# Optimization experiments

Measured on AMD Instinct MI355X. Metric: run time of the kernel, lower is better.

Reference implementation:

```python
import jax, jax.numpy as jnp
import numpy as np

B = 16384    # batch of game states
HAND = 8     # max_hand_size
A = 30       # max_actions
C = 4        # max cards per action combo
E = 32       # card_embed_dim
HID = 128    # hidden_dim


def _encode_cards(cards, val_emb, suit_emb, type_emb):
    # cards: int array, 0 = padding, 53 = joker (treated as padding for value/suit)
    invalid = (cards == 0) | (cards == 53)
    values = jnp.where(invalid, 0, (cards - 1) % 13 + 1)
    suits = jnp.where(invalid, 0, (cards - 1) // 13 + 1)
    ce = jnp.concatenate([val_emb[values], suit_emb[suits]], axis=-1)  # [..., E]
    ct = jnp.where(values == 11, 1, jnp.where(values == 12, 2, jnp.where(values == 13, 3, 0)))
    te = type_emb[ct]  # [..., 8]
    pad = jnp.zeros(te.shape[:-1] + (E - te.shape[-1],), ce.dtype)
    return ce + jnp.concatenate([te, pad], axis=-1)


def _mha(q, kv, wq, bq, wk, bk, wv, bv, wo, bo, nh, kpm=None):
    b, sq, e = q.shape
    sk = kv.shape[1]
    hd = e // nh
    Q = (q @ wq + bq).reshape(b, sq, nh, hd)
    K = (kv @ wk + bk).reshape(b, sk, nh, hd)
    V = (kv @ wv + bv).reshape(b, sk, nh, hd)
    s = jnp.einsum('bqhd,bkhd->bhqk', Q, K) * (1.0 / np.sqrt(hd))
    if kpm is not None:  # kpm True = valid key
        s = s + jnp.where(kpm[:, None, None, :], 0.0, -1e9)
    a = jax.nn.softmax(s, axis=-1)
    o = jnp.einsum('bhqk,bkhd->bqhd', a, V).reshape(b, sq, e)
    return o @ wo + bo


def _combo_features(cards):
    # cards: [A, C] int, 0 = padding. Vectorized version of _compute_combo_features.
    mask = cards != 0
    combo_size = mask.sum(1).astype(jnp.float32)
    values = jnp.where(mask, (cards - 1) % 13 + 1, 0)
    has_valid = mask.any(1)
    fidx = jnp.argmax(mask, axis=1)
    fv = values[jnp.arange(cards.shape[0]), fidx]  # first valid value per action
    same = jnp.where(mask, values == fv[:, None], True).all(1).astype(jnp.float32)
    vf = values.astype(jnp.float32)
    attack = jnp.where(values == 1, 1.0,
             jnp.where(values == 11, 10.0,
             jnp.where(values == 12, 15.0,
             jnp.where(values == 13, 20.0, vf))))
    total = (attack * mask).sum(1)
    suits = jnp.where(mask, (cards - 1) // 13 + 1, 0)
    uniq = jnp.stack([(suits == s).any(1) for s in (1, 2, 3, 4)], 0).sum(0).astype(jnp.float32)
    ace = ((values == 1) & mask).any(1).astype(jnp.float32)
    valid = ((combo_size <= 4.0) & ((same > 0) | (ace > 0))).astype(jnp.float32)
    feats = jnp.stack([combo_size, same, total, uniq, ace, valid], axis=1)  # [A, 6]
    return jnp.where(has_valid[:, None], feats, 0.0), has_valid


def _forward(hand_cards, enemy_card, hand_size, game_state, discard_pile_cards,
             action_card_indices, num_valid_actions,
             val_emb, suit_emb, type_emb,
             ce_w1, ce_b1, ce_w2, ce_b2,
             ha_wq, ha_bq, ha_wk, ha_bk, ha_wv, ha_bv, ha_wo, ha_bo,
             he_wq, he_bq, he_wk, he_bk, he_wv, he_bv, he_wo, he_bo,
             se_w1, se_b1, se_w2, se_b2,
             atc_w1, atc_b1, atc_w2, atc_b2,
             as_w1, as_b1, as_w2, as_b2, as_w3, as_b3,
             cx_w1, cx_b1, cx_w2, cx_b2, cx_w3, cx_b3):
    relu = jax.nn.relu
    hand_emb = _encode_cards(hand_cards, val_emb, suit_emb, type_emb)            # [B, HAND, E]
    enemy_emb = _encode_cards(enemy_card[:, None], val_emb, suit_emb, type_emb)  # [B, 1, E]
    hand_mask = hand_cards != 0
    attended = _mha(hand_emb, hand_emb, ha_wq, ha_bq, ha_wk, ha_bk, ha_wv, ha_bv, ha_wo, ha_bo, 8, kpm=hand_mask)
    ctx_he = _mha(attended, enemy_emb, he_wq, he_bq, he_wk, he_bk, he_wv, he_bv, he_wo, he_bo, 4)
    lengths = jnp.maximum(hand_size.astype(jnp.float32), 1.0)[:, None]
    hand_ctx = ctx_he.sum(1) / lengths                                           # [B, E]

    # strategic features (batched per game state)
    hvals = jnp.where(hand_cards == 0, 0, (hand_cards - 1) % 13 + 1)
    hsz = hand_size.astype(jnp.float32)
    aces = (hvals == 1).sum(1).astype(jnp.float32)
    faces = ((hvals >= 11) & (hvals <= 13)).sum(1).astype(jnp.float32)
    low = ((hvals >= 2) & (hvals <= 6)).sum(1).astype(jnp.float32)
    hsuits = jnp.where(hand_cards == 0, 0, (hand_cards - 1) // 13 + 1)
    scnt = [(hsuits == s).sum(1).astype(jnp.float32) for s in (1, 2, 3, 4)]
    hvr = faces / (hsz + 1e-8)
    sdiv = jnp.stack([(hsuits == s).any(1) for s in (1, 2, 3, 4)], 0).sum(0).astype(jnp.float32) / 4.0
    strat = jnp.stack([hsz, aces, faces, low, scnt[0], scnt[1], scnt[2], scnt[3], hvr, sdiv], axis=1)
    strat_in = jnp.concatenate([game_state, strat], axis=1)                      # [B, 20]
    strat_ctx = relu(strat_in @ se_w1 + se_b1) @ se_w2 + se_b2                   # [B, 32]

    combined = jnp.concatenate([hand_ctx, enemy_emb[:, 0], strat_ctx, discard_pile_cards], axis=1)  # [B, 150]
    h = relu(combined @ cx_w1 + cx_b1)
    h = relu(h @ cx_w2 + cx_b2)
    ctx = h @ cx_w3 + cx_b3                                                      # [B, HID]
    type_probs = jax.nn.softmax(relu(ctx @ atc_w1 + atc_b1) @ atc_w2 + atc_b2, axis=-1)  # [B, 4]

    feats, has_valid = _combo_features(action_card_indices)                      # [A, 6], [A]
    emb = _encode_cards(action_card_indices, val_emb, suit_emb, type_emb)        # [A, C, E]
    m = (action_card_indices != 0).astype(emb.dtype)[..., None]
    cnt = jnp.maximum(m.sum(1), 1.0)
    act_emb = (emb * m).sum(1) / cnt                                             # masked mean over real cards
    act_emb = jnp.where(has_valid[:, None], act_emb, 0.0)
    combo_enc = relu(feats @ ce_w1 + ce_b1) @ ce_w2 + ce_b2                      # [A, 16]

    Bn = ctx.shape[0]
    af = jnp.concatenate([
        jnp.broadcast_to(ctx[:, None, :], (Bn, A, HID)),
        jnp.broadcast_to(act_emb[None], (Bn, A, E)),
        jnp.broadcast_to(combo_enc[None], (Bn, A, 16)),
    ], axis=-1)                                                                  # [B, A, 176]
    s = relu(af @ as_w1 + as_b1)
    s = relu(s @ as_w2 + as_b2)
    score = (s @ as_w3 + as_b3)[..., 0]                                          # [B, A]

    strength = feats[:, 2] / 20.0                                                # [A]
    bonus_valid = type_probs[:, 0:1] * strength[None, :] + type_probs[:, 1:2] * (1.0 - strength[None, :])
    bonus_empty = jnp.broadcast_to(type_probs[:, 3:4] * 2.0, (Bn, A))
    bonus = jnp.where(has_valid[None, :], bonus_valid, bonus_empty)
    return score + bonus                                                          # [B, A]


def setup_inputs() -> dict:
    key = jax.random.key(0)
    ki = iter(jax.random.split(key, 64))
    def nrm(shape, s):
        return (s * jax.random.normal(next(ki), shape)).astype(jnp.float32)
    def lin(i, o, s=0.08):
        return nrm((i, o), s), nrm((o,), 0.02)
    d = {}
    hc = jax.random.randint(next(ki), (B, HAND), 0, 53)
    d['hand_cards'] = hc.at[:, 0].set(jax.random.randint(next(ki), (B,), 1, 53))  # at least one valid card per hand
    d['enemy_card'] = jax.random.randint(next(ki), (B,), 1, 53)
    d['hand_size'] = jax.random.randint(next(ki), (B,), 1, 9)
    d['game_state'] = nrm((B, 10), 1.0)
    d['discard_pile_cards'] = jax.random.uniform(next(ki), (B, 54), dtype=jnp.float32)
    d['action_card_indices'] = jax.random.randint(next(ki), (A, C), 1, 53)
    d['num_valid_actions'] = A
    d['val_emb'] = nrm((14, 16), 0.1).at[0].set(0.0)   # padding_idx=0
    d['suit_emb'] = nrm((5, 16), 0.1).at[0].set(0.0)   # padding_idx=0
    d['type_emb'] = nrm((4, 8), 0.1)
    d['ce_w1'], d['ce_b1'] = lin(6, 32)
    d['ce_w2'], d['ce_b2'] = lin(32, 16)
    for p in ('ha', 'he'):
        for t in ('q', 'k', 'v', 'o'):
            d[p + '_w' + t], d[p + '_b' + t] = lin(E, E)
    d['se_w1'], d['se_b1'] = lin(20, 64)
    d['se_w2'], d['se_b2'] = lin(64, 32)
    d['atc_w1'], d['atc_b1'] = lin(HID, 64)
    d['atc_w2'], d['atc_b2'] = lin(64, 4)
    d['as_w1'], d['as_b1'] = lin(HID + E + 16, 64)
    d['as_w2'], d['as_b2'] = lin(64, 32)
    d['as_w3'], d['as_b3'] = lin(32, 1)
    d['cx_w1'], d['cx_b1'] = lin(2 * E + 32 + 54, HID)
    d['cx_w2'], d['cx_b2'] = lin(HID, HID)
    d['cx_w3'], d['cx_b3'] = lin(HID, HID)
    return d


def reference(hand_cards, enemy_card, hand_size, game_state, discard_pile_cards,
              action_card_indices, num_valid_actions,
              val_emb, suit_emb, type_emb,
              ce_w1, ce_b1, ce_w2, ce_b2,
              ha_wq, ha_bq, ha_wk, ha_bk, ha_wv, ha_bv, ha_wo, ha_bo,
              he_wq, he_bq, he_wk, he_bk, he_wv, he_bv, he_wo, he_bo,
              se_w1, se_b1, se_w2, se_b2,
              atc_w1, atc_b1, atc_w2, atc_b2,
              as_w1, as_b1, as_w2, as_b2, as_w3, as_b3,
              cx_w1, cx_b1, cx_w2, cx_b2, cx_w3, cx_b3):
    return _forward(hand_cards, enemy_card, hand_size, game_state, discard_pile_cards,
                    action_card_indices, num_valid_actions,
                    val_emb, suit_emb, type_emb,
                    ce_w1, ce_b1, ce_w2, ce_b2,
                    ha_wq, ha_bq, ha_wk, ha_bk, ha_wv, ha_bv, ha_wo, ha_bo,
                    he_wq, he_bq, he_wk, he_bk, he_wv, he_bv, he_wo, he_bo,
                    se_w1, se_b1, se_w2, se_b2,
                    atc_w1, atc_b1, atc_w2, atc_b2,
                    as_w1, as_b1, as_w2, as_b2, as_w3, as_b3,
                    cx_w1, cx_b1, cx_w2, cx_b2, cx_w3, cx_b3)
```

## Files before the change

kernel.cpp:

```cpp
#include <hip/hip_runtime.h>
#include <math.h>


__device__ __forceinline__ void encode_card32(int c,
                                              const float* __restrict__ val_emb,
                                              const float* __restrict__ suit_emb,
                                              const float* __restrict__ type_emb,
                                              float* e) {
  bool inv = (c == 0) || (c == 53);
  int v = inv ? 0 : ((c - 1) % 13 + 1);
  int s = inv ? 0 : ((c - 1) / 13 + 1);
  int ct = (v == 11) ? 1 : (v == 12) ? 2 : (v == 13) ? 3 : 0;
#pragma unroll
  for (int i = 0; i < 16; ++i) e[i] = val_emb[v * 16 + i];
#pragma unroll
  for (int i = 0; i < 16; ++i) e[16 + i] = suit_emb[s * 16 + i];
#pragma unroll
  for (int i = 0; i < 8; ++i) e[i] += type_emb[ct * 8 + i];
}

__global__ __launch_bounds__(64) void action_kernel(
    const int* __restrict__ acards,
    const float* __restrict__ val_emb, const float* __restrict__ suit_emb,
    const float* __restrict__ type_emb,
    const float* __restrict__ ce_w1, const float* __restrict__ ce_b1,
    const float* __restrict__ ce_w2, const float* __restrict__ ce_b2,
    const float* __restrict__ as_w1, const float* __restrict__ as_b1,
    float* __restrict__ ws) {
  __shared__ float sAct[30][32];
  __shared__ float sCombo[30][16];
  const int tid = threadIdx.x;

  if (tid < 30) {
    int c[4];
#pragma unroll
    for (int i = 0; i < 4; ++i) c[i] = acards[tid * 4 + i];
    bool mask[4]; int vals[4], suits[4]; int csize = 0; bool hasv = false;
#pragma unroll
    for (int i = 0; i < 4; ++i) {
      mask[i] = (c[i] != 0);
      if (mask[i]) { csize++; hasv = true; }
      vals[i] = mask[i] ? ((c[i] - 1) % 13 + 1) : 0;
      suits[i] = mask[i] ? ((c[i] - 1) / 13 + 1) : 0;
    }
    int fvv = mask[0] ? vals[0] : mask[1] ? vals[1] : mask[2] ? vals[2]
              : mask[3] ? vals[3] : vals[0];
    bool same = true;
#pragma unroll
    for (int i = 0; i < 4; ++i) if (mask[i] && vals[i] != fvv) same = false;
    float total = 0.f;
#pragma unroll
    for (int i = 0; i < 4; ++i) {
      if (mask[i]) {
        int v = vals[i];
        total += (v == 1) ? 1.f : (v == 11) ? 10.f : (v == 12) ? 15.f
                 : (v == 13) ? 20.f : (float)v;
      }
    }
    float uniq = 0.f;
#pragma unroll
    for (int s = 1; s <= 4; ++s) {
      bool any = false;
#pragma unroll
      for (int i = 0; i < 4; ++i) if (suits[i] == s) any = true;
      uniq += any ? 1.f : 0.f;
    }
    bool ace = false;
#pragma unroll
    for (int i = 0; i < 4; ++i) if (mask[i] && vals[i] == 1) ace = true;
    float f_same = same ? 1.f : 0.f, f_ace = ace ? 1.f : 0.f;
    float valid = (((float)csize <= 4.f) && (f_same > 0.f || f_ace > 0.f)) ? 1.f : 0.f;
    float feats[6] = {(float)csize, f_same, total, uniq, f_ace, valid};
    if (!hasv) { for (int i = 0; i < 6; ++i) feats[i] = 0.f; }
    float emb[32];
#pragma unroll
    for (int i = 0; i < 32; ++i) emb[i] = 0.f;
    float cnt = 0.f;
#pragma unroll
    for (int i = 0; i < 4; ++i) {
      float e[32];
      encode_card32(c[i], val_emb, suit_emb, type_emb, e);
      if (mask[i]) {
#pragma unroll
        for (int j = 0; j < 32; ++j) emb[j] += e[j];
        cnt += 1.f;
      }
    }
    float invc = 1.f / fmaxf(cnt, 1.f);
#pragma unroll
    for (int j = 0; j < 32; ++j) sAct[tid][j] = hasv ? emb[j] * invc : 0.f;
    float t32[32];
#pragma unroll
    for (int j = 0; j < 32; ++j) {
      float acc = ce_b1[j];
#pragma unroll
      for (int k = 0; k < 6; ++k) acc += feats[k] * ce_w1[k * 32 + j];
      t32[j] = fmaxf(acc, 0.f);
    }
#pragma unroll
    for (int j = 0; j < 16; ++j) {
      float acc = ce_b2[j];
#pragma unroll
      for (int k = 0; k < 32; ++k) acc += t32[k] * ce_w2[k * 16 + j];
      sCombo[tid][j] = acc;
    }
    ws[1920 + tid] = total * 0.05f;
    ws[1950 + tid] = hasv ? 1.f : 0.f;
  }
  __syncthreads();
  for (int idx = tid; idx < 1920; idx += 64) {
    int a = idx >> 6, j = idx & 63;
    float acc = as_b1[j];
#pragma unroll
    for (int k = 0; k < 32; ++k) acc += sAct[a][k] * as_w1[(128 + k) * 64 + j];
#pragma unroll
    for (int k = 0; k < 16; ++k) acc += sCombo[a][k] * as_w1[(160 + k) * 64 + j];
    ws[idx] = acc;
  }
}

template <int K, int NJ, bool RELU, bool HASB>
__device__ __forceinline__ void layerT(
    const float* __restrict__ inB, float* __restrict__ outB,
    const float* __restrict__ W, int ldw, int j0,
    const float* __restrict__ bias, int r) {
  float acc[NJ];
#pragma unroll
  for (int j = 0; j < NJ; ++j) acc[j] = HASB ? bias[j0 + j] : 0.f;
#pragma unroll 4
  for (int k = 0; k < K; ++k) {
    float a = inB[k * 64 + r];
    const float* wr = W + (size_t)k * ldw + j0;
#pragma unroll
    for (int j = 0; j < NJ; ++j) acc[j] += a * wr[j];
  }
#pragma unroll
  for (int j = 0; j < NJ; ++j)
    outB[(j0 + j) * 64 + r] = RELU ? fmaxf(acc[j], 0.f) : acc[j];
}

__global__ __launch_bounds__(1024) void policy_main(
    const int* __restrict__ hand_cards, const int* __restrict__ enemy_card,
    const int* __restrict__ hand_size, const float* __restrict__ game_state,
    const float* __restrict__ discard,
    const float* __restrict__ val_emb, const float* __restrict__ suit_emb,
    const float* __restrict__ type_emb,
    const float* __restrict__ he_wv, const float* __restrict__ he_bv,
    const float* __restrict__ he_wo, const float* __restrict__ he_bo,
    const float* __restrict__ se_w1, const float* __restrict__ se_b1,
    const float* __restrict__ se_w2, const float* __restrict__ se_b2,
    const float* __restrict__ atc_w1, const float* __restrict__ atc_b1,
    const float* __restrict__ atc_w2, const float* __restrict__ atc_b2,
    const float* __restrict__ as_w1,
    const float* __restrict__ as_w2, const float* __restrict__ as_b2,
    const float* __restrict__ as_w3, const float* __restrict__ as_b3,
    const float* __restrict__ cx_w1, const float* __restrict__ cx_b1,
    const float* __restrict__ cx_w2, const float* __restrict__ cx_b2,
    const float* __restrict__ cx_w3, const float* __restrict__ cx_b3,
    const float* __restrict__ ws, float* __restrict__ out) {
  __shared__ float bufA[128 * 64];
  __shared__ float bufB[128 * 64];

  const int tid = threadIdx.x;
  const int r = tid & 63;
  const int wq = __builtin_amdgcn_readfirstlane(tid >> 6);
  const int b0 = blockIdx.x * 64;

  if (wq == 2) {
#pragma unroll
    for (int k = 0; k < 10; ++k)
      bufB[k * 64 + r] = game_state[(size_t)(b0 + r) * 10 + k];
  }
  if (wq == 0) {
    const int b = b0 + r;
    const float hsz = (float)hand_size[b];
    int aces = 0, faces = 0, low = 0, c1 = 0, c2 = 0, c3 = 0, c4 = 0;
#pragma unroll
    for (int i = 0; i < 8; ++i) {
      int c = hand_cards[b * 8 + i];
      int v = (c == 0) ? 0 : ((c - 1) % 13 + 1);
      int s = (c == 0) ? 0 : ((c - 1) / 13 + 1);
      aces += (v == 1);
      faces += (v >= 11 && v <= 13);
      low += (v >= 2 && v <= 6);
      c1 += (s == 1); c2 += (s == 2); c3 += (s == 3); c4 += (s == 4);
    }
    float sdiv = (float)((c1 > 0) + (c2 > 0) + (c3 > 0) + (c4 > 0)) * 0.25f;
    float hvr = (float)faces / (hsz + 1e-8f);
    bufB[(10 + 0) * 64 + r] = hsz;          bufB[(10 + 1) * 64 + r] = (float)aces;
    bufB[(10 + 2) * 64 + r] = (float)faces; bufB[(10 + 3) * 64 + r] = (float)low;
    bufB[(10 + 4) * 64 + r] = (float)c1;    bufB[(10 + 5) * 64 + r] = (float)c2;
    bufB[(10 + 6) * 64 + r] = (float)c3;    bufB[(10 + 7) * 64 + r] = (float)c4;
    bufB[(10 + 8) * 64 + r] = hvr;          bufB[(10 + 9) * 64 + r] = sdiv;
  }
  if (wq == 1) {
    const int b = b0 + r;
    bufB[116 * 64 + r] = 8.0f / fmaxf((float)hand_size[b], 1.0f);
    float e[32];
    encode_card32(enemy_card[b], val_emb, suit_emb, type_emb, e);
#pragma unroll
    for (int i = 0; i < 32; ++i) bufA[(32 + i) * 64 + r] = e[i];
  }
  __syncthreads();

  layerT<20, 4, true, true>(bufB, bufB + 20 * 64, se_w1, 64, wq * 4, se_b1, r);
  __syncthreads();

  layerT<64, 2, false, true>(bufB + 20 * 64, bufA + 64 * 64, se_w2, 32, wq * 2, se_b2, r);
  layerT<32, 2, false, true>(bufA + 32 * 64, bufB + 84 * 64, he_wv, 32, wq * 2, he_bv, r);
  __syncthreads();

  {
    const int j0 = wq * 2;
    float acc[2] = {he_bo[j0], he_bo[j0 + 1]};
#pragma unroll 4
    for (int k = 0; k < 32; ++k) {
      float a = bufB[(84 + k) * 64 + r];
      const float* wr = he_wo + (size_t)k * 32 + j0;
      acc[0] += a * wr[0];
      acc[1] += a * wr[1];
    }
    float scale = bufB[116 * 64 + r];
    bufA[(j0 + 0) * 64 + r] = scale * acc[0];
    bufA[(j0 + 1) * 64 + r] = scale * acc[1];
  }
  __syncthreads();

  {
    const int j0 = wq * 8;
    float acc[8];
#pragma unroll
    for (int j = 0; j < 8; ++j) acc[j] = cx_b1[j0 + j];
#pragma unroll 4
    for (int k = 0; k < 96; ++k) {
      float a = bufA[k * 64 + r];
      const float* wr = cx_w1 + (size_t)k * 128 + j0;
#pragma unroll
      for (int j = 0; j < 8; ++j) acc[j] += a * wr[j];
    }
    const float* drow = discard + (size_t)(b0 + r) * 54;
#pragma unroll 2
    for (int k = 0; k < 54; ++k) {
      float a = drow[k];
      const float* wr = cx_w1 + (size_t)(96 + k) * 128 + j0;
#pragma unroll
      for (int j = 0; j < 8; ++j) acc[j] += a * wr[j];
    }
    __syncthreads();
#pragma unroll
    for (int j = 0; j < 8; ++j) bufB[(j0 + j) * 64 + r] = fmaxf(acc[j], 0.f);
  }
  __syncthreads();

  layerT<128, 8, true, true>(bufB, bufA, cx_w2, 128, wq * 8, cx_b2, r);
  __syncthreads();

  layerT<128, 8, false, true>(bufA, bufB, cx_w3, 128, wq * 8, cx_b3, r);
  __syncthreads();

  if (wq < 8) {
    layerT<128, 8, true, true>(bufB, bufA, atc_w1, 64, wq * 8, atc_b1, r);
  } else {
    layerT<128, 8, false, false>(bufB, bufA + 64 * 64, as_w1, 64, (wq - 8) * 8,
                                 nullptr, r);
  }
  __syncthreads();

  if (wq < 4) {
    float acc = atc_b2[wq];
#pragma unroll 4
    for (int k = 0; k < 64; ++k) acc += bufA[k * 64 + r] * atc_w2[k * 4 + wq];
    bufB[wq * 64 + r] = acc;
  }
  __syncthreads();

  if (wq < 15) {
    float l0 = bufB[0 * 64 + r], l1 = bufB[1 * 64 + r];
    float l2 = bufB[2 * 64 + r], l3 = bufB[3 * 64 + r];
    float m = fmaxf(fmaxf(l0, l1), fmaxf(l2, l3));
    float e0 = expf(l0 - m), e1 = expf(l1 - m), e2 = expf(l2 - m), e3 = expf(l3 - m);
    float inv = 1.f / (e0 + e1 + e2 + e3);
    float tp0 = e0 * inv, tp1 = e1 * inv, tp3 = e3 * inv;

    const float b3v = as_b3[0];
#pragma unroll 1
    for (int i = 0; i < 2; ++i) {
      const int a = wq * 2 + i;
      const float* qa = ws + a * 64;
      float acc[32];
#pragma unroll
      for (int j = 0; j < 32; ++j) acc[j] = 0.f;
#pragma unroll 1
      for (int seg = 0; seg < 4; ++seg) {
        float p[16];
#pragma unroll
        for (int kk = 0; kk < 16; ++kk)
          p[kk] = bufA[(64 + seg * 16 + kk) * 64 + r];
#pragma unroll
        for (int kk = 0; kk < 16; ++kk) {
          float s = fmaxf(p[kk] + qa[seg * 16 + kk], 0.f);
          const float* w2r = as_w2 + (size_t)(seg * 16 + kk) * 32;
#pragma unroll
          for (int j = 0; j < 32; ++j) acc[j] += s * w2r[j];
        }
      }
      float sc = b3v;
#pragma unroll
      for (int j = 0; j < 32; ++j)
        sc += fmaxf(acc[j] + as_b2[j], 0.f) * as_w3[j];
      float st = ws[1920 + a], hv = ws[1950 + a];
      float bon = (hv > 0.5f) ? (tp0 * st + tp1 * (1.f - st)) : tp3 * 2.f;
      out[(size_t)(b0 + r) * 30 + a] = sc + bon;
    }
  }
}

extern "C" void kernel_launch(void* const* d_in, const int* in_sizes, int n_in,
                              void* d_out, int out_size, void* d_ws, size_t ws_size,
                              hipStream_t stream) {
  (void)in_sizes; (void)n_in; (void)out_size; (void)ws_size;
  const int* hand_cards = (const int*)d_in[0];
  const int* enemy_card = (const int*)d_in[1];
  const int* hand_size = (const int*)d_in[2];
  const float* game_state = (const float*)d_in[3];
  const float* discard = (const float*)d_in[4];
  const int* acards = (const int*)d_in[5];
  const float* val_emb = (const float*)d_in[7];
  const float* suit_emb = (const float*)d_in[8];
  const float* type_emb = (const float*)d_in[9];
  const float* ce_w1 = (const float*)d_in[10], * ce_b1 = (const float*)d_in[11];
  const float* ce_w2 = (const float*)d_in[12], * ce_b2 = (const float*)d_in[13];
  const float* he_wv = (const float*)d_in[26], * he_bv = (const float*)d_in[27];
  const float* he_wo = (const float*)d_in[28], * he_bo = (const float*)d_in[29];
  const float* se_w1 = (const float*)d_in[30], * se_b1 = (const float*)d_in[31];
  const float* se_w2 = (const float*)d_in[32], * se_b2 = (const float*)d_in[33];
  const float* atc_w1 = (const float*)d_in[34], * atc_b1 = (const float*)d_in[35];
  const float* atc_w2 = (const float*)d_in[36], * atc_b2 = (const float*)d_in[37];
  const float* as_w1 = (const float*)d_in[38], * as_b1 = (const float*)d_in[39];
  const float* as_w2 = (const float*)d_in[40], * as_b2 = (const float*)d_in[41];
  const float* as_w3 = (const float*)d_in[42], * as_b3 = (const float*)d_in[43];
  const float* cx_w1 = (const float*)d_in[44], * cx_b1 = (const float*)d_in[45];
  const float* cx_w2 = (const float*)d_in[46], * cx_b2 = (const float*)d_in[47];
  const float* cx_w3 = (const float*)d_in[48], * cx_b3 = (const float*)d_in[49];
  float* ws = (float*)d_ws;
  float* out = (float*)d_out;

  hipLaunchKernelGGL(action_kernel, dim3(1), dim3(64), 0, stream,
                     acards, val_emb, suit_emb, type_emb,
                     ce_w1, ce_b1, ce_w2, ce_b2, as_w1, as_b1, ws);
  hipLaunchKernelGGL(policy_main, dim3(256), dim3(1024), 0, stream,
                     hand_cards, enemy_card, hand_size, game_state, discard,
                     val_emb, suit_emb, type_emb,
                     he_wv, he_bv, he_wo, he_bo,
                     se_w1, se_b1, se_w2, se_b2,
                     atc_w1, atc_b1, atc_w2, atc_b2,
                     as_w1, as_w2, as_b2, as_w3, as_b3,
                     cx_w1, cx_b1, cx_w2, cx_b2, cx_w3, cx_b3,
                     ws, out);
}
```

Baseline: 259.4 us.

## Store activations in quad-interleaved shared layout for float4 LDS access

Changes the shared-memory activation buffers from column-major [col][row] to a quad-interleaved layout, so each thread reads and writes four consecutive features as one float4. The aim is fewer LDS instructions in the MLP layers and the scoring loop. It also removes one barrier inside the cx layer-1 block and tidies the accumulator code. The cost is 16-byte LDS accesses, which may bring bank-conflict or alignment trade-offs, and more complex indexing that has to stay consistent across every stage.

```diff
diff --git a/kernel.cpp b/kernel.cpp
--- a/kernel.cpp
+++ b/kernel.cpp
@@ -1,6 +1,8 @@
 #include <hip/hip_runtime.h>
 #include <math.h>
 
+
+#define QOFF(c, r) ((((c) >> 2) * 256) + ((r) * 4) + ((c) & 3))
 
 __device__ __forceinline__ void encode_card32(int c,
                                               const float* __restrict__ val_emb,
@@ -119,24 +121,52 @@
   }
 }
 
-template <int K, int NJ, bool RELU, bool HASB>
-__device__ __forceinline__ void layerT(
-    const float* __restrict__ inB, float* __restrict__ outB,
-    const float* __restrict__ W, int ldw, int j0,
+template <int K, int NJ, bool RELU, bool HASB, bool QIN, bool QOUT>
+__device__ __forceinline__ void layerU(
+    const float* __restrict__ in, int inColBase, float* __restrict__ outB,
+    int outColBase, const float* __restrict__ W, int ldw, int j0,
     const float* __restrict__ bias, int r) {
   float acc[NJ];
 #pragma unroll
   for (int j = 0; j < NJ; ++j) acc[j] = HASB ? bias[j0 + j] : 0.f;
+  if constexpr (QIN) {
+    static_assert(K % 4 == 0, "quad input needs K%4==0");
+    const int g0 = inColBase >> 2;
 #pragma unroll 4
-  for (int k = 0; k < K; ++k) {
-    float a = inB[k * 64 + r];
-    const float* wr = W + (size_t)k * ldw + j0;
-#pragma unroll
-    for (int j = 0; j < NJ; ++j) acc[j] += a * wr[j];
-  }
-#pragma unroll
-  for (int j = 0; j < NJ; ++j)
-    outB[(j0 + j) * 64 + r] = RELU ? fmaxf(acc[j], 0.f) : acc[j];
+    for (int g = 0; g < K / 4; ++g) {
+      float4 a = *(const float4*)&in[(g0 + g) * 256 + r * 4];
+#pragma unroll
+      for (int q = 0; q < 4; ++q) {
+        float av = (q == 0) ? a.x : (q == 1) ? a.y : (q == 2) ? a.z : a.w;
+        const float* wr = W + (size_t)(g * 4 + q) * ldw + j0;
+#pragma unroll
+        for (int j = 0; j < NJ; ++j) acc[j] += av * wr[j];
+      }
+    }
+  } else {
+#pragma unroll 4
+    for (int k = 0; k < K; ++k) {
+      float a = in[(inColBase + k) * 64 + r];
+      const float* wr = W + (size_t)k * ldw + j0;
+#pragma unroll
+      for (int j = 0; j < NJ; ++j) acc[j] += a * wr[j];
+    }
+  }
+#pragma unroll
+  for (int j = 0; j < NJ; ++j) if (RELU) acc[j] = fmaxf(acc[j], 0.f);
+  if constexpr (QOUT && NJ == 8) {
+    const int c0 = outColBase + j0;
+    float4 o0 = make_float4(acc[0], acc[1], acc[2], acc[3]);
+    float4 o1 = make_float4(acc[4], acc[5], acc[6], acc[7]);
+    *(float4*)&outB[(c0 >> 2) * 256 + r * 4] = o0;
+    *(float4*)&outB[((c0 >> 2) + 1) * 256 + r * 4] = o1;
+  } else if constexpr (QOUT) {
+#pragma unroll
+    for (int j = 0; j < NJ; ++j) outB[QOFF(outColBase + j0 + j, r)] = acc[j];
+  } else {
+#pragma unroll
+    for (int j = 0; j < NJ; ++j) outB[(outColBase + j0 + j) * 64 + r] = acc[j];
+  }
 }
 
 __global__ __launch_bounds__(1024) void policy_main(
@@ -199,30 +229,36 @@
     float e[32];
     encode_card32(enemy_card[b], val_emb, suit_emb, type_emb, e);
 #pragma unroll
-    for (int i = 0; i < 32; ++i) bufA[(32 + i) * 64 + r] = e[i];
-  }
-  __syncthreads();
-
-  layerT<20, 4, true, true>(bufB, bufB + 20 * 64, se_w1, 64, wq * 4, se_b1, r);
-  __syncthreads();
-
-  layerT<64, 2, false, true>(bufB + 20 * 64, bufA + 64 * 64, se_w2, 32, wq * 2, se_b2, r);
-  layerT<32, 2, false, true>(bufA + 32 * 64, bufB + 84 * 64, he_wv, 32, wq * 2, he_bv, r);
+    for (int g = 0; g < 8; ++g) {
+      float4 ev = make_float4(e[g * 4], e[g * 4 + 1], e[g * 4 + 2], e[g * 4 + 3]);
+      *(float4*)&bufA[(8 + g) * 256 + r * 4] = ev;
+    }
+  }
+  __syncthreads();
+
+  layerU<20, 4, true, true, false, false>(bufB, 0, bufB, 20, se_w1, 64, wq * 4,
+                                          se_b1, r);
+  __syncthreads();
+
+  layerU<64, 2, false, true, false, true>(bufB, 20, bufA, 64, se_w2, 32, wq * 2,
+                                          se_b2, r);
+  layerU<32, 2, false, true, true, false>(bufA, 32, bufB, 84, he_wv, 32, wq * 2,
+                                          he_bv, r);
   __syncthreads();
 
   {
     const int j0 = wq * 2;
-    float acc[2] = {he_bo[j0], he_bo[j0 + 1]};
+    float acc0 = he_bo[j0], acc1 = he_bo[j0 + 1];
 #pragma unroll 4
     for (int k = 0; k < 32; ++k) {
       float a = bufB[(84 + k) * 64 + r];
       const float* wr = he_wo + (size_t)k * 32 + j0;
-      acc[0] += a * wr[0];
-      acc[1] += a * wr[1];
+      acc0 += a * wr[0];
+      acc1 += a * wr[1];
     }
     float scale = bufB[116 * 64 + r];
-    bufA[(j0 + 0) * 64 + r] = scale * acc[0];
-    bufA[(j0 + 1) * 64 + r] = scale * acc[1];
+    bufA[QOFF(j0, r)] = scale * acc0;
+    bufA[QOFF(j0 + 1, r)] = scale * acc1;
   }
   __syncthreads();
 
@@ -232,11 +268,15 @@
 #pragma unroll
     for (int j = 0; j < 8; ++j) acc[j] = cx_b1[j0 + j];
 #pragma unroll 4
-    for (int k = 0; k < 96; ++k) {
-      float a = bufA[k * 64 + r];
-      const float* wr = cx_w1 + (size_t)k * 128 + j0;
-#pragma unroll
-      for (int j = 0; j < 8; ++j) acc[j] += a * wr[j];
+    for (int g = 0; g < 24; ++g) {
+      float4 a = *(const float4*)&bufA[g * 256 + r * 4];
+#pragma unroll
+      for (int q = 0; q < 4; ++q) {
+        float av = (q == 0) ? a.x : (q == 1) ? a.y : (q == 2) ? a.z : a.w;
+        const float* wr = cx_w1 + (size_t)(g * 4 + q) * 128 + j0;
+#pragma unroll
+        for (int j = 0; j < 8; ++j) acc[j] += av * wr[j];
+      }
     }
     const float* drow = discard + (size_t)(b0 + r) * 54;
 #pragma unroll 2
@@ -246,30 +286,42 @@
 #pragma unroll
       for (int j = 0; j < 8; ++j) acc[j] += a * wr[j];
     }
-    __syncthreads();
-#pragma unroll
-    for (int j = 0; j < 8; ++j) bufB[(j0 + j) * 64 + r] = fmaxf(acc[j], 0.f);
-  }
-  __syncthreads();
-
-  layerT<128, 8, true, true>(bufB, bufA, cx_w2, 128, wq * 8, cx_b2, r);
-  __syncthreads();
-
-  layerT<128, 8, false, true>(bufA, bufB, cx_w3, 128, wq * 8, cx_b3, r);
+    float4 o0 = make_float4(fmaxf(acc[0], 0.f), fmaxf(acc[1], 0.f),
+                            fmaxf(acc[2], 0.f), fmaxf(acc[3], 0.f));
+    float4 o1 = make_float4(fmaxf(acc[4], 0.f), fmaxf(acc[5], 0.f),
+                            fmaxf(acc[6], 0.f), fmaxf(acc[7], 0.f));
+    *(float4*)&bufB[(j0 >> 2) * 256 + r * 4] = o0;
+    *(float4*)&bufB[((j0 >> 2) + 1) * 256 + r * 4] = o1;
+  }
+  __syncthreads();
+
+  layerU<128, 8, true, true, true, true>(bufB, 0, bufA, 0, cx_w2, 128, wq * 8,
+                                         cx_b2, r);
+  __syncthreads();
+
+  layerU<128, 8, false, true, true, true>(bufA, 0, bufB, 0, cx_w3, 128, wq * 8,
+                                          cx_b3, r);
   __syncthreads();
 
   if (wq < 8) {
-    layerT<128, 8, true, true>(bufB, bufA, atc_w1, 64, wq * 8, atc_b1, r);
+    layerU<128, 8, true, true, true, true>(bufB, 0, bufA, 0, atc_w1, 64, wq * 8,
+                                           atc_b1, r);
   } else {
-    layerT<128, 8, false, false>(bufB, bufA + 64 * 64, as_w1, 64, (wq - 8) * 8,
-                                 nullptr, r);
+    layerU<128, 8, false, false, true, true>(bufB, 0, bufA, 64, as_w1, 64,
+                                             (wq - 8) * 8, nullptr, r);
   }
   __syncthreads();
 
   if (wq < 4) {
     float acc = atc_b2[wq];
 #pragma unroll 4
-    for (int k = 0; k < 64; ++k) acc += bufA[k * 64 + r] * atc_w2[k * 4 + wq];
+    for (int g = 0; g < 16; ++g) {
+      float4 t = *(const float4*)&bufA[g * 256 + r * 4];
+      acc += t.x * atc_w2[(g * 4 + 0) * 4 + wq];
+      acc += t.y * atc_w2[(g * 4 + 1) * 4 + wq];
+      acc += t.z * atc_w2[(g * 4 + 2) * 4 + wq];
+      acc += t.w * atc_w2[(g * 4 + 3) * 4 + wq];
+    }
     bufB[wq * 64 + r] = acc;
   }
   __syncthreads();
@@ -290,16 +342,15 @@
       float acc[32];
 #pragma unroll
       for (int j = 0; j < 32; ++j) acc[j] = 0.f;
-#pragma unroll 1
-      for (int seg = 0; seg < 4; ++seg) {
-        float p[16];
-#pragma unroll
-        for (int kk = 0; kk < 16; ++kk)
-          p[kk] = bufA[(64 + seg * 16 + kk) * 64 + r];
-#pragma unroll
-        for (int kk = 0; kk < 16; ++kk) {
-          float s = fmaxf(p[kk] + qa[seg * 16 + kk], 0.f);
-          const float* w2r = as_w2 + (size_t)(seg * 16 + kk) * 32;
+#pragma unroll 2
+      for (int g = 0; g < 16; ++g) {
+        float4 pv = *(const float4*)&bufA[(16 + g) * 256 + r * 4];
+#pragma unroll
+        for (int q = 0; q < 4; ++q) {
+          float p = (q == 0) ? pv.x : (q == 1) ? pv.y : (q == 2) ? pv.z : pv.w;
+          const int k = g * 4 + q;
+          float s = fmaxf(p + qa[k], 0.f);
+          const float* w2r = as_w2 + (size_t)k * 32;
 #pragma unroll
           for (int j = 0; j < 32; ++j) acc[j] += s * w2r[j];
         }
```

After: 244.1 us. 5.9% less time.
